# Performance work log

Measured on AMD Instinct MI355X. Metric: run time of the kernel, lower is better.

Reference implementation:

```python
import jax, jax.numpy as jnp
import numpy as np

HID = 32
NUM_GRAPHS = 256
N_NODES = 100000


def graph_conv(x, src, dst, ew, rel_w, rel_b, root_w):
    # PyG GraphConv: out = lin_rel(sum_{j in N(i)} e_ji * x_j) + lin_root(x_i)
    msg = x[src] * ew[:, None]                                  # [E, F] gather
    agg = jax.ops.segment_sum(msg, dst, num_segments=N_NODES)    # [N, F] scatter-add
    return agg @ rel_w + rel_b + x @ root_w


def setup_inputs() -> dict:
    key = jax.random.key(0)
    ks = jax.random.split(key, 16)
    N, E, F = N_NODES, 1600000, 64
    x = jax.random.normal(ks[0], (N, F), dtype=jnp.float32)
    edge_index = jax.random.randint(ks[1], (2, E), 0, N, dtype=jnp.int64)
    edge_attr = jax.random.uniform(ks[2], (E,), dtype=jnp.float32)
    batch = jnp.sort(jax.random.randint(ks[3], (N,), 0, NUM_GRAPHS, dtype=jnp.int64))
    s = lambda k, shp: jax.random.normal(k, shp, dtype=jnp.float32) * 0.1
    return {
        "x": x, "edge_index": edge_index, "edge_attr": edge_attr, "batch": batch,
        "conv1_rel_w": s(ks[4], (F, HID)), "conv1_rel_b": jnp.zeros((HID,), jnp.float32),
        "conv1_root_w": s(ks[5], (F, HID)),
        "conv2_rel_w": s(ks[6], (HID, HID)), "conv2_rel_b": jnp.zeros((HID,), jnp.float32),
        "conv2_root_w": s(ks[7], (HID, HID)),
        "lin1_w": s(ks[8], (HID, 32)), "lin1_b": jnp.zeros((32,), jnp.float32),
        "lin2_w": s(ks[9], (32, 16)), "lin2_b": jnp.zeros((16,), jnp.float32),
        "lin_w": s(ks[10], (16, 1)), "lin_b": jnp.zeros((1,), jnp.float32),
    }


def reference(x, edge_index, edge_attr, batch,
              conv1_rel_w, conv1_rel_b, conv1_root_w,
              conv2_rel_w, conv2_rel_b, conv2_root_w,
              lin1_w, lin1_b, lin2_w, lin2_b, lin_w, lin_b):
    src, dst = edge_index[0], edge_index[1]
    h = jax.nn.relu(graph_conv(x, src, dst, edge_attr, conv1_rel_w, conv1_rel_b, conv1_root_w))
    h = jax.nn.relu(graph_conv(h, src, dst, edge_attr, conv2_rel_w, conv2_rel_b, conv2_root_w))
    # global mean pool over graphs
    sums = jax.ops.segment_sum(h, batch, num_segments=NUM_GRAPHS)          # [G, 32]
    cnts = jax.ops.segment_sum(jnp.ones((h.shape[0],), h.dtype), batch, num_segments=NUM_GRAPHS)
    g = sums / jnp.maximum(cnts, 1.0)[:, None]
    # dropout is identity in eval mode
    g = jax.nn.relu(g @ lin1_w + lin1_b)
    g = g @ lin2_w + lin2_b
    g = jax.nn.relu(g)
    return g @ lin_w + lin_b  # [G, 1]
```

## Files before the change

kernel.cpp:

```cpp
#include <hip/hip_runtime.h>
#include <hip/hip_fp16.h>

#define NGRAPH 256
#define FIN 64
#define HID 32
#define NB_SHIFT 8
#define NB_NODES 256
#define KMAX2 512
#define EPB 2048
#define EPT 8
#define NT 64
#define XPAD 65
#define HPAD 33

__global__ __launch_bounds__(256, 4) void node_lin64(
    const float* __restrict__ x, const float* __restrict__ Wrel,
    const float* __restrict__ Wroot, const float* __restrict__ bias,
    __half* __restrict__ A, float* __restrict__ B, int N)
{
    __shared__ float sWr[FIN * HID];
    __shared__ float sWo[FIN * HID];
    __shared__ float sb[HID];
    __shared__ float sx[NT * XPAD];
    int tid = threadIdx.x;
    {
        const float4* Wr4 = (const float4*)Wrel;
        const float4* Wo4 = (const float4*)Wroot;
        for (int i = tid; i < FIN * HID / 4; i += 256) {
            ((float4*)sWr)[i] = Wr4[i];
            ((float4*)sWo)[i] = Wo4[i];
        }
        if (tid < HID) sb[tid] = bias[tid];
    }
    int base = blockIdx.x * NT;
    {
        const float4* x4 = (const float4*)x;
        for (int i = tid; i < NT * 16; i += 256) {
            int row = i >> 4, c4 = i & 15;
            int n = base + row;
            float4 v = (n < N) ? x4[(size_t)n * 16 + c4]
                               : make_float4(0.f, 0.f, 0.f, 0.f);
            *(float4*)&sx[row * XPAD + c4 * 4] = v;
        }
    }
    __syncthreads();

    int nl = tid >> 3;
    int fq = (tid & 7) * 4;
    const float* xa = &sx[nl * XPAD];
    const float* xb = &sx[(nl + 32) * XPAD];
    float4 ar0 = make_float4(0.f,0.f,0.f,0.f), ao0 = ar0;
    float4 ar1 = ar0, ao1 = ar0;
    #pragma unroll 4
    for (int k = 0; k < FIN; ++k) {
        float4 w4 = *(const float4*)&sWr[k * HID + fq];
        float4 o4 = *(const float4*)&sWo[k * HID + fq];
        float va = xa[k], vb = xb[k];
        ar0.x = fmaf(va, w4.x, ar0.x); ar0.y = fmaf(va, w4.y, ar0.y);
        ar0.z = fmaf(va, w4.z, ar0.z); ar0.w = fmaf(va, w4.w, ar0.w);
        ao0.x = fmaf(va, o4.x, ao0.x); ao0.y = fmaf(va, o4.y, ao0.y);
        ao0.z = fmaf(va, o4.z, ao0.z); ao0.w = fmaf(va, o4.w, ao0.w);
        ar1.x = fmaf(vb, w4.x, ar1.x); ar1.y = fmaf(vb, w4.y, ar1.y);
        ar1.z = fmaf(vb, w4.z, ar1.z); ar1.w = fmaf(vb, w4.w, ar1.w);
        ao1.x = fmaf(vb, o4.x, ao1.x); ao1.y = fmaf(vb, o4.y, ao1.y);
        ao1.z = fmaf(vb, o4.z, ao1.z); ao1.w = fmaf(vb, o4.w, ao1.w);
    }
    float4 bb = *(const float4*)&sb[fq];
    int n0 = base + nl, n1 = base + nl + 32;
    if (n0 < N) {
        __half2 pa = __floats2half2_rn(ar0.x, ar0.y);
        __half2 pb = __floats2half2_rn(ar0.z, ar0.w);
        uint2 pk; pk.x = *(unsigned*)&pa; pk.y = *(unsigned*)&pb;
        *(uint2*)&A[(size_t)n0 * HID + fq] = pk;
        ao0.x += bb.x; ao0.y += bb.y; ao0.z += bb.z; ao0.w += bb.w;
        *(float4*)&B[(size_t)n0 * HID + fq] = ao0;
    }
    if (n1 < N) {
        __half2 pa = __floats2half2_rn(ar1.x, ar1.y);
        __half2 pb = __floats2half2_rn(ar1.z, ar1.w);
        uint2 pk; pk.x = *(unsigned*)&pa; pk.y = *(unsigned*)&pb;
        *(uint2*)&A[(size_t)n1 * HID + fq] = pk;
        ao1.x += bb.x; ao1.y += bb.y; ao1.z += bb.z; ao1.w += bb.w;
        *(float4*)&B[(size_t)n1 * HID + fq] = ao1;
    }
}

__global__ __launch_bounds__(256, 4) void node_lin32(
    const float* __restrict__ Hpre, const float* __restrict__ Wrel,
    const float* __restrict__ Wroot, const float* __restrict__ bias,
    __half* __restrict__ A, float* __restrict__ C, int N)
{
    __shared__ float sWr[HID * HID];
    __shared__ float sWo[HID * HID];
    __shared__ float sb[HID];
    __shared__ float sh[NT * HPAD];
    int tid = threadIdx.x;
    {
        const float4* Wr4 = (const float4*)Wrel;
        const float4* Wo4 = (const float4*)Wroot;
        for (int i = tid; i < HID * HID / 4; i += 256) {
            ((float4*)sWr)[i] = Wr4[i];
            ((float4*)sWo)[i] = Wo4[i];
        }
        if (tid < HID) sb[tid] = bias[tid];
    }
    int base = blockIdx.x * NT;
    {
        const float4* H4 = (const float4*)Hpre;
        for (int i = tid; i < NT * 8; i += 256) {
            int row = i >> 3, c4 = i & 7;
            int n = base + row;
            float4 v = make_float4(0.f, 0.f, 0.f, 0.f);
            if (n < N) {
                v = H4[(size_t)n * 8 + c4];
                v.x = v.x > 0.f ? v.x : 0.f; v.y = v.y > 0.f ? v.y : 0.f;
                v.z = v.z > 0.f ? v.z : 0.f; v.w = v.w > 0.f ? v.w : 0.f;
            }
            *(float4*)&sh[row * HPAD + c4 * 4] = v;
        }
    }
    __syncthreads();

    int nl = tid >> 3;
    int fq = (tid & 7) * 4;
    const float* xa = &sh[nl * HPAD];
    const float* xb = &sh[(nl + 32) * HPAD];
    float4 ar0 = make_float4(0.f,0.f,0.f,0.f), ao0 = ar0;
    float4 ar1 = ar0, ao1 = ar0;
    #pragma unroll 4
    for (int k = 0; k < HID; ++k) {
        float4 w4 = *(const float4*)&sWr[k * HID + fq];
        float4 o4 = *(const float4*)&sWo[k * HID + fq];
        float va = xa[k], vb = xb[k];
        ar0.x = fmaf(va, w4.x, ar0.x); ar0.y = fmaf(va, w4.y, ar0.y);
        ar0.z = fmaf(va, w4.z, ar0.z); ar0.w = fmaf(va, w4.w, ar0.w);
        ao0.x = fmaf(va, o4.x, ao0.x); ao0.y = fmaf(va, o4.y, ao0.y);
        ao0.z = fmaf(va, o4.z, ao0.z); ao0.w = fmaf(va, o4.w, ao0.w);
        ar1.x = fmaf(vb, w4.x, ar1.x); ar1.y = fmaf(vb, w4.y, ar1.y);
        ar1.z = fmaf(vb, w4.z, ar1.z); ar1.w = fmaf(vb, w4.w, ar1.w);
        ao1.x = fmaf(vb, o4.x, ao1.x); ao1.y = fmaf(vb, o4.y, ao1.y);
        ao1.z = fmaf(vb, o4.z, ao1.z); ao1.w = fmaf(vb, o4.w, ao1.w);
    }
    float4 bb = *(const float4*)&sb[fq];
    int n0 = base + nl, n1 = base + nl + 32;
    if (n0 < N) {
        __half2 pa = __floats2half2_rn(ar0.x, ar0.y);
        __half2 pb = __floats2half2_rn(ar0.z, ar0.w);
        uint2 pk; pk.x = *(unsigned*)&pa; pk.y = *(unsigned*)&pb;
        *(uint2*)&A[(size_t)n0 * HID + fq] = pk;
        ao0.x += bb.x; ao0.y += bb.y; ao0.z += bb.z; ao0.w += bb.w;
        *(float4*)&C[(size_t)n0 * HID + fq] = ao0;
    }
    if (n1 < N) {
        __half2 pa = __floats2half2_rn(ar1.x, ar1.y);
        __half2 pb = __floats2half2_rn(ar1.z, ar1.w);
        uint2 pk; pk.x = *(unsigned*)&pa; pk.y = *(unsigned*)&pb;
        *(uint2*)&A[(size_t)n1 * HID + fq] = pk;
        ao1.x += bb.x; ao1.y += bb.y; ao1.z += bb.z; ao1.w += bb.w;
        *(float4*)&C[(size_t)n1 * HID + fq] = ao1;
    }
}


__global__ __launch_bounds__(256) void bucket_hist(
    const int* __restrict__ dst, int* __restrict__ cbb, int E, int K, int NBLK)
{
    __shared__ int h[KMAX2];
    int tid = threadIdx.x;
    for (int i = tid; i < K; i += 256) h[i] = 0;
    __syncthreads();
    int e0 = blockIdx.x * EPB + tid * 8;
    if (e0 + 7 < E) {
        int4 d0 = *reinterpret_cast<const int4*>(dst + e0);
        int4 d1 = *reinterpret_cast<const int4*>(dst + e0 + 4);
        atomicAdd(&h[d0.x >> NB_SHIFT], 1); atomicAdd(&h[d0.y >> NB_SHIFT], 1);
        atomicAdd(&h[d0.z >> NB_SHIFT], 1); atomicAdd(&h[d0.w >> NB_SHIFT], 1);
        atomicAdd(&h[d1.x >> NB_SHIFT], 1); atomicAdd(&h[d1.y >> NB_SHIFT], 1);
        atomicAdd(&h[d1.z >> NB_SHIFT], 1); atomicAdd(&h[d1.w >> NB_SHIFT], 1);
    } else {
        for (int e = e0; e < E && e < e0 + 8; ++e)
            atomicAdd(&h[dst[e] >> NB_SHIFT], 1);
    }
    __syncthreads();
    for (int i = tid; i < K; i += 256)
        cbb[(size_t)i * NBLK + blockIdx.x] = h[i];
}

__global__ __launch_bounds__(256) void bucket_scan(
    int* __restrict__ cbb, int* __restrict__ btot, int NBLK)
{
    __shared__ int sc[256];
    size_t row = (size_t)blockIdx.x * NBLK;
    int t = threadIdx.x;
    int base = t * 4;
    int v[4]; int s = 0;
    #pragma unroll
    for (int j = 0; j < 4; ++j) { v[j] = (base + j < NBLK) ? cbb[row + base + j] : 0; s += v[j]; }
    sc[t] = s;
    __syncthreads();
    int acc = s;
    for (int off = 1; off < 256; off <<= 1) {
        int add = (t >= off) ? sc[t - off] : 0;
        __syncthreads();
        acc += add;
        sc[t] = acc;
        __syncthreads();
    }
    int run = acc - s;
    #pragma unroll
    for (int j = 0; j < 4; ++j) {
        if (base + j < NBLK) cbb[row + base + j] = run;
        run += v[j];
    }
    if (t == 255) btot[blockIdx.x] = acc;
}

__global__ __launch_bounds__(256) void btot_scan(
    const int* __restrict__ btot, int* __restrict__ bbase, int K)
{
    __shared__ int sc[256];
    int t = threadIdx.x;
    int base = t * 4;
    int v[4]; int s = 0;
    #pragma unroll
    for (int j = 0; j < 4; ++j) { v[j] = (base + j < K) ? btot[base + j] : 0; s += v[j]; }
    sc[t] = s;
    __syncthreads();
    int acc = s;
    for (int off = 1; off < 256; off <<= 1) {
        int add = (t >= off) ? sc[t - off] : 0;
        __syncthreads();
        acc += add;
        sc[t] = acc;
        __syncthreads();
    }
    int run = acc - s;
    #pragma unroll
    for (int j = 0; j < 4; ++j) {
        if (base + j < K) bbase[base + j] = run;
        run += v[j];
    }
    if (t == 255) bbase[K] = acc;
}

__global__ __launch_bounds__(256) void partB(
    const int* __restrict__ src, const int* __restrict__ dst,
    const float* __restrict__ ew, const int* __restrict__ cbb,
    const int* __restrict__ bbase, int2* __restrict__ stg8,
    int E, int K, int NBLK)
{
    __shared__ int4 pay[EPB];
    __shared__ int h[KMAX2];
    __shared__ int lofs[KMAX2];
    __shared__ int gb[KMAX2];
    __shared__ int sc[256];
    int tid = threadIdx.x;
    for (int i = tid; i < K; i += 256) h[i] = 0;
    __syncthreads();

    int base = blockIdx.x * EPB;
    int es[EPT], ds[EPT]; float wsr[EPT];
    #pragma unroll
    for (int k = 0; k < EPT; ++k) {
        int e = base + k * 256 + tid;
        if (e < E) {
            es[k] = src[e]; ds[k] = dst[e]; wsr[k] = ew[e];
            atomicAdd(&h[ds[k] >> NB_SHIFT], 1);
        } else ds[k] = -1;
    }
    __syncthreads();

    int b0 = tid * 2;
    int v0 = (b0 < K) ? h[b0] : 0;
    int v1 = (b0 + 1 < K) ? h[b0 + 1] : 0;
    int s = v0 + v1;
    sc[tid] = s;
    __syncthreads();
    int acc = s;
    for (int off = 1; off < 256; off <<= 1) {
        int add = (tid >= off) ? sc[tid - off] : 0;
        __syncthreads();
        acc += add;
        sc[tid] = acc;
        __syncthreads();
    }
    int run = acc - s;
    if (b0 < K) lofs[b0] = run;
    if (b0 + 1 < K) lofs[b0 + 1] = run + v0;
    __syncthreads();

    for (int b = tid; b < K; b += 256) {
        gb[b] = bbase[b] + cbb[(size_t)b * NBLK + blockIdx.x];
        h[b] = lofs[b];
    }
    __syncthreads();

    #pragma unroll
    for (int k = 0; k < EPT; ++k) {
        if (ds[k] >= 0) {
            int b = ds[k] >> NB_SHIFT;
            int dloc = ds[k] & (NB_NODES - 1);
            int slot = atomicAdd(&h[b], 1);
            pay[slot] = make_int4(es[k] | (dloc << 17), __float_as_int(wsr[k]),
                                  gb[b] + slot - lofs[b], 0);
        }
    }
    __syncthreads();

    int tot = E - base; if (tot > EPB) tot = EPB;
    for (int i = tid; i < tot; i += 256) {
        int4 p = pay[i];
        stg8[p.z] = make_int2(p.x, p.y);
    }
}

__global__ __launch_bounds__(512) void partC2(
    const int2* __restrict__ stg8, const int* __restrict__ bbase,
    int* __restrict__ rowptr, int2* __restrict__ perm, int N, int K)
{
    __shared__ int hcnt[NB_NODES];
    __shared__ int hinc[NB_NODES];
    int b = blockIdx.x;
    int n0 = b << NB_SHIFT;
    int nTop = n0 + NB_NODES; if (nTop > N) nTop = N;
    int nloc = nTop - n0;
    int tid = threadIdx.x;
    if (tid < NB_NODES) hcnt[tid] = 0;
    __syncthreads();
    int lo = bbase[b], hi = bbase[b + 1];
    for (int e = lo + tid; e < hi; e += 512)
        atomicAdd(&hcnt[stg8[e].x >> 17], 1);
    __syncthreads();
    if (tid < NB_NODES) hinc[tid] = hcnt[tid];
    __syncthreads();
    for (int off = 1; off < NB_NODES; off <<= 1) {
        int v = (tid < NB_NODES && tid >= off) ? hinc[tid - off] : 0;
        __syncthreads();
        if (tid < NB_NODES) hinc[tid] += v;
        __syncthreads();
    }
    if (tid < nloc) {
        int excl = hinc[tid] - hcnt[tid];
        rowptr[n0 + tid] = lo + excl;
        hcnt[tid] = excl;
    }
    if (b == K - 1 && tid == 0) rowptr[N] = hi;
    __syncthreads();
    for (int e = lo + tid; e < hi; e += 512) {
        int2 p = stg8[e];
        int pos = lo + atomicAdd(&hcnt[p.x >> 17], 1);
        perm[pos] = make_int2(p.x & 0x1FFFF, p.y);
    }
}

__global__ __launch_bounds__(256) void csr_agg(
    const int* __restrict__ rowptr, const int2* __restrict__ perm,
    const __half* __restrict__ A, float* __restrict__ out, int N)
{
    int gid = blockIdx.x * 256 + threadIdx.x;
    int n = gid >> 6;
    if (n >= N) return;
    int lane = threadIdx.x & 63;
    int slot = lane >> 3;
    int q = lane & 7;
    int e0 = rowptr[n], e1 = rowptr[n + 1];
    const uint2* A2 = (const uint2*)A;
    float4 a0 = make_float4(0.f, 0.f, 0.f, 0.f);
    float4 a1 = make_float4(0.f, 0.f, 0.f, 0.f);
    int e = e0 + slot;
    for (; e + 8 < e1; e += 16) {
        int2 p0 = perm[e];
        int2 p1 = perm[e + 8];
        uint2 r0 = A2[(size_t)p0.x * 8 + q];
        uint2 r1 = A2[(size_t)p1.x * 8 + q];
        float w0 = __int_as_float(p0.y), w1 = __int_as_float(p1.y);
        float2 f01 = __half22float2(*(__half2*)&r0.x);
        float2 f23 = __half22float2(*(__half2*)&r0.y);
        float2 g01 = __half22float2(*(__half2*)&r1.x);
        float2 g23 = __half22float2(*(__half2*)&r1.y);
        a0.x = fmaf(f01.x, w0, a0.x); a0.y = fmaf(f01.y, w0, a0.y);
        a0.z = fmaf(f23.x, w0, a0.z); a0.w = fmaf(f23.y, w0, a0.w);
        a1.x = fmaf(g01.x, w1, a1.x); a1.y = fmaf(g01.y, w1, a1.y);
        a1.z = fmaf(g23.x, w1, a1.z); a1.w = fmaf(g23.y, w1, a1.w);
    }
    for (; e < e1; e += 8) {
        int2 p = perm[e];
        uint2 r = A2[(size_t)p.x * 8 + q];
        float w = __int_as_float(p.y);
        float2 f01 = __half22float2(*(__half2*)&r.x);
        float2 f23 = __half22float2(*(__half2*)&r.y);
        a0.x = fmaf(f01.x, w, a0.x); a0.y = fmaf(f01.y, w, a0.y);
        a0.z = fmaf(f23.x, w, a0.z); a0.w = fmaf(f23.y, w, a0.w);
    }
    a0.x += a1.x; a0.y += a1.y; a0.z += a1.z; a0.w += a1.w;
    #pragma unroll
    for (int off = 8; off < 64; off <<= 1) {
        a0.x += __shfl_xor(a0.x, off, 64);
        a0.y += __shfl_xor(a0.y, off, 64);
        a0.z += __shfl_xor(a0.z, off, 64);
        a0.w += __shfl_xor(a0.w, off, 64);
    }
    if (lane < 8) {
        float4* O4 = (float4*)out;
        size_t oi = (size_t)n * 8 + q;
        float4 o = O4[oi];
        o.x += a0.x; o.y += a0.y; o.z += a0.z; o.w += a0.w;
        O4[oi] = o;
    }
}

__global__ __launch_bounds__(256) void pool_mlp(
    const float* __restrict__ C, const int* __restrict__ batch, int N,
    const float* __restrict__ W1, const float* __restrict__ b1,
    const float* __restrict__ W2, const float* __restrict__ b2,
    const float* __restrict__ W3, const float* __restrict__ b3,
    float* __restrict__ out)
{
    int g = blockIdx.x;
    int tid = threadIdx.x;
    int lo, hi;
    {
        int l = 0, r = N;
        while (l < r) { int m = (l + r) >> 1; if (batch[m] < g) l = m + 1; else r = m; }
        lo = l;
        r = N;
        while (l < r) { int m = (l + r) >> 1; if (batch[m] < g + 1) l = m + 1; else r = m; }
        hi = l;
    }
    __shared__ float ssum[8][32];
    __shared__ float gvec[32];
    __shared__ float h1v[32];
    __shared__ float h2v[16];
    int f = tid & 31, seg = tid >> 5;
    float acc = 0.f;
    for (int n = lo + seg; n < hi; n += 8) {
        float v = C[(size_t)n * HID + f];
        acc += v > 0.f ? v : 0.f;
    }
    ssum[seg][f] = acc;
    __syncthreads();
    if (tid < 32) {
        float s = 0.f;
        #pragma unroll
        for (int k = 0; k < 8; ++k) s += ssum[k][tid];
        float c = (float)(hi - lo); c = c > 1.f ? c : 1.f;
        gvec[tid] = s / c;
    }
    __syncthreads();
    if (tid < 32) {
        float a = b1[tid];
        #pragma unroll
        for (int k = 0; k < 32; ++k) a = fmaf(gvec[k], W1[k * 32 + tid], a);
        h1v[tid] = a > 0.f ? a : 0.f;
    }
    __syncthreads();
    if (tid < 16) {
        float a = b2[tid];
        #pragma unroll
        for (int k = 0; k < 32; ++k) a = fmaf(h1v[k], W2[k * 16 + tid], a);
        h2v[tid] = a > 0.f ? a : 0.f;
    }
    __syncthreads();
    if (tid == 0) {
        float o = b3[0];
        #pragma unroll
        for (int k = 0; k < 16; ++k) o = fmaf(h2v[k], W3[k], o);
        out[g] = o;
    }
}

extern "C" void kernel_launch(void* const* d_in, const int* in_sizes, int n_in,
                              void* d_out, int out_size, void* d_ws, size_t ws_size,
                              hipStream_t stream) {
    const float* x     = (const float*)d_in[0];
    const int*   ei    = (const int*)d_in[1];
    const float* ew    = (const float*)d_in[2];
    const int*   batch = (const int*)d_in[3];
    const float* c1rw  = (const float*)d_in[4];
    const float* c1rb  = (const float*)d_in[5];
    const float* c1ow  = (const float*)d_in[6];
    const float* c2rw  = (const float*)d_in[7];
    const float* c2rb  = (const float*)d_in[8];
    const float* c2ow  = (const float*)d_in[9];
    const float* l1w   = (const float*)d_in[10];
    const float* l1b   = (const float*)d_in[11];
    const float* l2w   = (const float*)d_in[12];
    const float* l2b   = (const float*)d_in[13];
    const float* lw    = (const float*)d_in[14];
    const float* lb    = (const float*)d_in[15];

    int N = in_sizes[0] / FIN;
    int E = in_sizes[2];
    const int* src = ei;
    const int* dst = ei + E;
    int K    = (N + NB_NODES - 1) >> NB_SHIFT;
    int NBLK = (E + EPB - 1) / EPB;

    char* ws = (char*)d_ws;
    size_t off = 0;
    auto alloc = [&](size_t nbytes) { void* p = ws + off; off += (nbytes + 255) & ~size_t(255); return p; };
    __half* A     = (__half*)alloc((size_t)N * HID * 2);
    float*  BC    = (float*) alloc((size_t)N * HID * 4);
    int2*   perm  = (int2*)  alloc((size_t)E * 8);
    int*   rowptr = (int*)   alloc((size_t)(N + 1) * 4);
    int*   btot   = (int*)   alloc((size_t)KMAX2 * 4);
    int*   bbase  = (int*)   alloc((size_t)(KMAX2 + 1) * 4);
    int*   cbb    = (int*)A;
    int2*  stg8   = (int2*)BC;

    int nb_node = (N + NT - 1) / NT;
    int nb_agg  = (int)(((long long)N * 64 + 255) / 256);

    bucket_hist<<<NBLK, 256, 0, stream>>>(dst, cbb, E, K, NBLK);
    bucket_scan<<<K, 256, 0, stream>>>(cbb, btot, NBLK);
    btot_scan<<<1, 256, 0, stream>>>(btot, bbase, K);
    partB<<<NBLK, 256, 0, stream>>>(src, dst, ew, cbb, bbase, stg8, E, K, NBLK);
    partC2<<<K, 512, 0, stream>>>(stg8, bbase, rowptr, perm, N, K);

    node_lin64<<<nb_node, 256, 0, stream>>>(x, c1rw, c1ow, c1rb, A, BC, N);
    csr_agg<<<nb_agg, 256, 0, stream>>>(rowptr, perm, A, BC, N);
    node_lin32<<<nb_node, 256, 0, stream>>>(BC, c2rw, c2ow, c2rb, A, BC, N);
    csr_agg<<<nb_agg, 256, 0, stream>>>(rowptr, perm, A, BC, N);
    pool_mlp<<<NGRAPH, 256, 0, stream>>>(BC, batch, N, l1w, l1b, l2w, l2b, lw, lb,
                                         (float*)d_out);
}
```

Baseline: 173.4 us.

## Fuse bucket histogram with first node linear and stage buckets in LDS

Merges the bucket histogram kernel and the first-layer node linear transform into one launch, using block index ranges to pick the role and a shared-memory union. This removes one launch and lets the two independent stages run concurrently. Because of that, the scratch buffers cbb and stg8 get dedicated workspace instead of aliasing A/BC. In partC2, each bucket's edges are now loaded once into a 6016-entry shared buffer when they fit, so the counting and scatter passes read LDS instead of global memory twice. The cost is more LDS per block, which may lower partC2 occupancy.

Result: no change. 175.9 us (+1.4%).

```diff
diff --git a/kernel.cpp b/kernel.cpp
--- a/kernel.cpp
+++ b/kernel.cpp
@@ -12,27 +12,52 @@
 #define NT 64
 #define XPAD 65
 #define HPAD 33
-
-__global__ __launch_bounds__(256, 4) void node_lin64(
+#define PCAP 6016
+
+union SU {
+    int h[KMAX2];
+    struct { float Wr[FIN * HID]; float Wo[FIN * HID]; float b[HID];
+             float x[NT * XPAD]; } g;
+};
+
+__global__ __launch_bounds__(256, 4) void hist_lin64(
+    const int* __restrict__ dst, int* __restrict__ cbb, int E, int K, int NBLK,
     const float* __restrict__ x, const float* __restrict__ Wrel,
     const float* __restrict__ Wroot, const float* __restrict__ bias,
     __half* __restrict__ A, float* __restrict__ B, int N)
 {
-    __shared__ float sWr[FIN * HID];
-    __shared__ float sWo[FIN * HID];
-    __shared__ float sb[HID];
-    __shared__ float sx[NT * XPAD];
+    __shared__ SU u;
     int tid = threadIdx.x;
+    if (blockIdx.x < (unsigned)NBLK) {
+        for (int i = tid; i < K; i += 256) u.h[i] = 0;
+        __syncthreads();
+        int e0 = blockIdx.x * EPB + tid * 8;
+        if (e0 + 7 < E) {
+            int4 d0 = *reinterpret_cast<const int4*>(dst + e0);
+            int4 d1 = *reinterpret_cast<const int4*>(dst + e0 + 4);
+            atomicAdd(&u.h[d0.x >> NB_SHIFT], 1); atomicAdd(&u.h[d0.y >> NB_SHIFT], 1);
+            atomicAdd(&u.h[d0.z >> NB_SHIFT], 1); atomicAdd(&u.h[d0.w >> NB_SHIFT], 1);
+            atomicAdd(&u.h[d1.x >> NB_SHIFT], 1); atomicAdd(&u.h[d1.y >> NB_SHIFT], 1);
+            atomicAdd(&u.h[d1.z >> NB_SHIFT], 1); atomicAdd(&u.h[d1.w >> NB_SHIFT], 1);
+        } else {
+            for (int e = e0; e < E && e < e0 + 8; ++e)
+                atomicAdd(&u.h[dst[e] >> NB_SHIFT], 1);
+        }
+        __syncthreads();
+        for (int i = tid; i < K; i += 256)
+            cbb[(size_t)i * NBLK + blockIdx.x] = u.h[i];
+        return;
+    }
     {
         const float4* Wr4 = (const float4*)Wrel;
         const float4* Wo4 = (const float4*)Wroot;
         for (int i = tid; i < FIN * HID / 4; i += 256) {
-            ((float4*)sWr)[i] = Wr4[i];
-            ((float4*)sWo)[i] = Wo4[i];
-        }
-        if (tid < HID) sb[tid] = bias[tid];
-    }
-    int base = blockIdx.x * NT;
+            ((float4*)u.g.Wr)[i] = Wr4[i];
+            ((float4*)u.g.Wo)[i] = Wo4[i];
+        }
+        if (tid < HID) u.g.b[tid] = bias[tid];
+    }
+    int base = (blockIdx.x - NBLK) * NT;
     {
         const float4* x4 = (const float4*)x;
         for (int i = tid; i < NT * 16; i += 256) {
@@ -40,21 +65,21 @@
             int n = base + row;
             float4 v = (n < N) ? x4[(size_t)n * 16 + c4]
                                : make_float4(0.f, 0.f, 0.f, 0.f);
-            *(float4*)&sx[row * XPAD + c4 * 4] = v;
+            *(float4*)&u.g.x[row * XPAD + c4 * 4] = v;
         }
     }
     __syncthreads();
 
     int nl = tid >> 3;
     int fq = (tid & 7) * 4;
-    const float* xa = &sx[nl * XPAD];
-    const float* xb = &sx[(nl + 32) * XPAD];
+    const float* xa = &u.g.x[nl * XPAD];
+    const float* xb = &u.g.x[(nl + 32) * XPAD];
     float4 ar0 = make_float4(0.f,0.f,0.f,0.f), ao0 = ar0;
     float4 ar1 = ar0, ao1 = ar0;
     #pragma unroll 4
     for (int k = 0; k < FIN; ++k) {
-        float4 w4 = *(const float4*)&sWr[k * HID + fq];
-        float4 o4 = *(const float4*)&sWo[k * HID + fq];
+        float4 w4 = *(const float4*)&u.g.Wr[k * HID + fq];
+        float4 o4 = *(const float4*)&u.g.Wo[k * HID + fq];
         float va = xa[k], vb = xb[k];
         ar0.x = fmaf(va, w4.x, ar0.x); ar0.y = fmaf(va, w4.y, ar0.y);
         ar0.z = fmaf(va, w4.z, ar0.z); ar0.w = fmaf(va, w4.w, ar0.w);
@@ -65,7 +90,7 @@
         ao1.x = fmaf(vb, o4.x, ao1.x); ao1.y = fmaf(vb, o4.y, ao1.y);
         ao1.z = fmaf(vb, o4.z, ao1.z); ao1.w = fmaf(vb, o4.w, ao1.w);
     }
-    float4 bb = *(const float4*)&sb[fq];
+    float4 bb = *(const float4*)&u.g.b[fq];
     int n0 = base + nl, n1 = base + nl + 32;
     if (n0 < N) {
         __half2 pa = __floats2half2_rn(ar0.x, ar0.y);
@@ -162,30 +187,6 @@
 }
 
 
-__global__ __launch_bounds__(256) void bucket_hist(
-    const int* __restrict__ dst, int* __restrict__ cbb, int E, int K, int NBLK)
-{
-    __shared__ int h[KMAX2];
-    int tid = threadIdx.x;
-    for (int i = tid; i < K; i += 256) h[i] = 0;
-    __syncthreads();
-    int e0 = blockIdx.x * EPB + tid * 8;
-    if (e0 + 7 < E) {
-        int4 d0 = *reinterpret_cast<const int4*>(dst + e0);
-        int4 d1 = *reinterpret_cast<const int4*>(dst + e0 + 4);
-        atomicAdd(&h[d0.x >> NB_SHIFT], 1); atomicAdd(&h[d0.y >> NB_SHIFT], 1);
-        atomicAdd(&h[d0.z >> NB_SHIFT], 1); atomicAdd(&h[d0.w >> NB_SHIFT], 1);
-        atomicAdd(&h[d1.x >> NB_SHIFT], 1); atomicAdd(&h[d1.y >> NB_SHIFT], 1);
-        atomicAdd(&h[d1.z >> NB_SHIFT], 1); atomicAdd(&h[d1.w >> NB_SHIFT], 1);
-    } else {
-        for (int e = e0; e < E && e < e0 + 8; ++e)
-            atomicAdd(&h[dst[e] >> NB_SHIFT], 1);
-    }
-    __syncthreads();
-    for (int i = tid; i < K; i += 256)
-        cbb[(size_t)i * NBLK + blockIdx.x] = h[i];
-}
-
 __global__ __launch_bounds__(256) void bucket_scan(
     int* __restrict__ cbb, int* __restrict__ btot, int NBLK)
 {
@@ -318,6 +319,7 @@
     const int2* __restrict__ stg8, const int* __restrict__ bbase,
     int* __restrict__ rowptr, int2* __restrict__ perm, int N, int K)
 {
+    __shared__ int2 pe[PCAP];
     __shared__ int hcnt[NB_NODES];
     __shared__ int hinc[NB_NODES];
     int b = blockIdx.x;
@@ -326,10 +328,20 @@
     int nloc = nTop - n0;
     int tid = threadIdx.x;
     if (tid < NB_NODES) hcnt[tid] = 0;
-    __syncthreads();
     int lo = bbase[b], hi = bbase[b + 1];
-    for (int e = lo + tid; e < hi; e += 512)
-        atomicAdd(&hcnt[stg8[e].x >> 17], 1);
+    int sz = hi - lo;
+    bool fit = (sz <= PCAP);
+    if (fit) {
+        for (int i = tid; i < sz; i += 512) pe[i] = stg8[lo + i];
+    }
+    __syncthreads();
+    if (fit) {
+        for (int i = tid; i < sz; i += 512)
+            atomicAdd(&hcnt[pe[i].x >> 17], 1);
+    } else {
+        for (int e = lo + tid; e < hi; e += 512)
+            atomicAdd(&hcnt[stg8[e].x >> 17], 1);
+    }
     __syncthreads();
     if (tid < NB_NODES) hinc[tid] = hcnt[tid];
     __syncthreads();
@@ -346,10 +358,18 @@
     }
     if (b == K - 1 && tid == 0) rowptr[N] = hi;
     __syncthreads();
-    for (int e = lo + tid; e < hi; e += 512) {
-        int2 p = stg8[e];
-        int pos = lo + atomicAdd(&hcnt[p.x >> 17], 1);
-        perm[pos] = make_int2(p.x & 0x1FFFF, p.y);
+    if (fit) {
+        for (int i = tid; i < sz; i += 512) {
+            int2 p = pe[i];
+            int pos = lo + atomicAdd(&hcnt[p.x >> 17], 1);
+            perm[pos] = make_int2(p.x & 0x1FFFF, p.y);
+        }
+    } else {
+        for (int e = lo + tid; e < hi; e += 512) {
+            int2 p = stg8[e];
+            int pos = lo + atomicAdd(&hcnt[p.x >> 17], 1);
+            perm[pos] = make_int2(p.x & 0x1FFFF, p.y);
+        }
     }
 }
 
@@ -502,22 +522,22 @@
     __half* A     = (__half*)alloc((size_t)N * HID * 2);
     float*  BC    = (float*) alloc((size_t)N * HID * 4);
     int2*   perm  = (int2*)  alloc((size_t)E * 8);
+    int2*   stg8  = (int2*)  alloc((size_t)E * 8);
+    int*    cbb   = (int*)   alloc((size_t)K * NBLK * 4);
     int*   rowptr = (int*)   alloc((size_t)(N + 1) * 4);
     int*   btot   = (int*)   alloc((size_t)KMAX2 * 4);
     int*   bbase  = (int*)   alloc((size_t)(KMAX2 + 1) * 4);
-    int*   cbb    = (int*)A;
-    int2*  stg8   = (int2*)BC;
 
     int nb_node = (N + NT - 1) / NT;
     int nb_agg  = (int)(((long long)N * 64 + 255) / 256);
 
-    bucket_hist<<<NBLK, 256, 0, stream>>>(dst, cbb, E, K, NBLK);
+    hist_lin64<<<NBLK + nb_node, 256, 0, stream>>>(
+        dst, cbb, E, K, NBLK, x, c1rw, c1ow, c1rb, A, BC, N);
     bucket_scan<<<K, 256, 0, stream>>>(cbb, btot, NBLK);
     btot_scan<<<1, 256, 0, stream>>>(btot, bbase, K);
     partB<<<NBLK, 256, 0, stream>>>(src, dst, ew, cbb, bbase, stg8, E, K, NBLK);
     partC2<<<K, 512, 0, stream>>>(stg8, bbase, rowptr, perm, N, K);
 
-    node_lin64<<<nb_node, 256, 0, stream>>>(x, c1rw, c1ow, c1rb, A, BC, N);
     csr_agg<<<nb_agg, 256, 0, stream>>>(rowptr, perm, A, BC, N);
     node_lin32<<<nb_node, 256, 0, stream>>>(BC, c2rw, c2ow, c2rb, A, BC, N);
     csr_agg<<<nb_agg, 256, 0, stream>>>(rowptr, perm, A, BC, N);
```
